# Kernel optimization log

Measured on AMD Instinct MI355X. Metric: run time of the kernel, lower is better.

The kernel has to match this reference:

```python
import jax, jax.numpy as jnp
import numpy as np
from jax import lax

SEQ, F, H1, H2, B, WV, OBJ, REL, VOCAB = 33, 20480, 900, 900, 2, 100, 35, 82, 117


def setup_inputs() -> dict:
    key = jax.random.key(0)
    ks = jax.random.split(key, 17)
    s = lambda k, shape: jax.random.normal(k, shape, jnp.float32) * 0.02
    return dict(
        x=jax.random.normal(ks[0], (SEQ, B, F), jnp.float32),
        w_ih1=s(ks[1], (4 * H1, F)), w_hh1=s(ks[2], (4 * H1, H1)),
        b_ih1=s(ks[3], (4 * H1,)), b_hh1=s(ks[4], (4 * H1,)),
        w_ih2=s(ks[5], (SEQ, 4 * H2, H1 + WV)), w_hh2=s(ks[6], (SEQ, 4 * H2, H2)),
        b_ih2=s(ks[7], (SEQ, 4 * H2)), b_hh2=s(ks[8], (SEQ, 4 * H2)),
        w_obj1=s(ks[9], (OBJ, H2)), b_obj1=s(ks[10], (OBJ,)),
        w_rel=s(ks[11], (REL, H2)), b_rel=s(ks[12], (REL,)),
        w_obj2=s(ks[13], (OBJ, H2)), b_obj2=s(ks[14], (OBJ,)),
        embed=s(ks[15], (VOCAB, WV)),
    )


def lstm_cell(xt, h, c, w_ih, w_hh, b_ih, b_hh):
    # torch gate order: input, forget, cell(g), output
    gates = xt @ w_ih.T + h @ w_hh.T + b_ih + b_hh
    i, f, g, o = jnp.split(gates, 4, axis=-1)
    c = jax.nn.sigmoid(f) * c + jax.nn.sigmoid(i) * jnp.tanh(g)
    h = jax.nn.sigmoid(o) * jnp.tanh(c)
    return h, c


def reference(x, w_ih1, w_hh1, b_ih1, b_hh1, w_ih2, w_hh2, b_ih2, b_hh2,
              w_obj1, b_obj1, w_rel, b_rel, w_obj2, b_obj2, embed):
    batch = x.shape[1]
    # layer-1 LSTM over full sequence
    def step1(carry, xt):
        h, c = lstm_cell(xt, carry[0], carry[1], w_ih1, w_hh1, b_ih1, b_hh1)
        return (h, c), h
    h0 = jnp.zeros((batch, H1), x.dtype)
    _, out1 = lax.scan(step1, (h0, h0), x)  # [SEQ, B, H1]

    # layer-2: first SEQ-2 cells with zero word vector, distinct weights per step
    wv0 = jnp.zeros((batch, WV), x.dtype)
    def step2(carry, inp):
        xt, wih, whh, bih, bhh = inp
        h, c = lstm_cell(jnp.concatenate([xt, wv0], axis=1), carry[0], carry[1], wih, whh, bih, bhh)
        return (h, c), None
    h20 = jnp.zeros((batch, H2), x.dtype)
    (h2, c2), _ = lax.scan(step2, (h20, h20),
                           (out1[:SEQ - 2], w_ih2[:SEQ - 2], w_hh2[:SEQ - 2],
                            b_ih2[:SEQ - 2], b_hh2[:SEQ - 2]))

    obj1 = h2 @ w_obj1.T + b_obj1                      # [B, 35]
    wv = embed[jnp.argmax(obj1, axis=1)]               # [B, 100]
    h2, c2 = lstm_cell(jnp.concatenate([out1[SEQ - 2], wv], axis=1), h2, c2,
                       w_ih2[SEQ - 2], w_hh2[SEQ - 2], b_ih2[SEQ - 2], b_hh2[SEQ - 2])

    rel = h2 @ w_rel.T + b_rel                         # [B, 82]
    wv = embed[jnp.argmax(rel, axis=1) + OBJ]
    h2, c2 = lstm_cell(jnp.concatenate([out1[SEQ - 1], wv], axis=1), h2, c2,
                       w_ih2[SEQ - 1], w_hh2[SEQ - 1], b_ih2[SEQ - 1], b_hh2[SEQ - 1])

    obj2 = h2 @ w_obj2.T + b_obj2                      # [B, 35]
    return (obj1, rel, obj2)
```

## Files before the change

### kernel.cpp

```cpp
#include <hip/hip_runtime.h>

#define SEQn 33
#define Fn   20480
#define Hn   900
#define Bn   2
#define WVn  100
#define OBJn 35
#define RELn 82
#define G4n  3600
#define Mn   66
#define NBLK 225

#define KS1  16
#define KSL1 (Fn/KS1)
#define RB1  15
#define RPB1 240
#define NC1  (KSL1/32)
#define WSTR 40

typedef __attribute__((ext_vector_type(8))) short bf16x8;
typedef __attribute__((ext_vector_type(4))) float f32x4;

__device__ __forceinline__ float sigf(float v){ return 1.f/(1.f+expf(-v)); }
__device__ __forceinline__ float dot4(float4 a, float4 b){ return a.x*b.x+a.y*b.y+a.z*b.z+a.w*b.w; }
__device__ __forceinline__ float wred(float v){
  #pragma unroll
  for (int d = 32; d >= 1; d >>= 1) v += __shfl_xor(v, d, 64);
  return v;
}
__device__ __forceinline__ float gload(const float* p){
  return __hip_atomic_load((const float*)p, __ATOMIC_RELAXED, __HIP_MEMORY_SCOPE_AGENT);
}
__device__ __forceinline__ void gstore(float* p, float v){
  __hip_atomic_store(p, v, __ATOMIC_RELAXED, __HIP_MEMORY_SCOPE_AGENT);
}
__device__ __forceinline__ unsigned short f2bf(float f){
  unsigned u = __float_as_uint(f);
  unsigned r = u + 0x7FFFu + ((u >> 16) & 1u);
  return (unsigned short)(r >> 16);
}
__device__ __forceinline__ float bf2f(unsigned short h){
  return __uint_as_float(((unsigned)h) << 16);
}

__device__ __forceinline__ void gbar(unsigned* bar){
  __syncthreads();
  if (threadIdx.x == 0) {
    unsigned g = __hip_atomic_load(&bar[0], __ATOMIC_RELAXED, __HIP_MEMORY_SCOPE_AGENT);
    unsigned cnt = __hip_atomic_fetch_add(&bar[32], 1u, __ATOMIC_RELAXED, __HIP_MEMORY_SCOPE_AGENT);
    if (cnt == (unsigned)(NBLK-1)) {
      __hip_atomic_store(&bar[32], 0u, __ATOMIC_RELAXED, __HIP_MEMORY_SCOPE_AGENT);
      asm volatile("s_waitcnt vmcnt(0)" ::: "memory");
      __hip_atomic_store(&bar[0], g+1u, __ATOMIC_RELAXED, __HIP_MEMORY_SCOPE_AGENT);
    } else {
      unsigned cur;
      do { __builtin_amdgcn_s_sleep(1);
           cur = __hip_atomic_load(&bar[0], __ATOMIC_RELAXED, __HIP_MEMORY_SCOPE_AGENT);
      } while (cur == g);
    }
  }
  __syncthreads();
}

__device__ __forceinline__ void gbar_lite(unsigned* bar, int wv){
  asm volatile("" ::: "memory");
  if (wv == 0) asm volatile("s_waitcnt vmcnt(0)" ::: "memory");
  __builtin_amdgcn_sched_barrier(0);
  __builtin_amdgcn_s_barrier();
  __builtin_amdgcn_sched_barrier(0);
  if (threadIdx.x == 0) {
    unsigned g = __hip_atomic_load(&bar[0], __ATOMIC_RELAXED, __HIP_MEMORY_SCOPE_AGENT);
    unsigned cnt = __hip_atomic_fetch_add(&bar[32], 1u, __ATOMIC_RELAXED, __HIP_MEMORY_SCOPE_AGENT);
    if (cnt == (unsigned)(NBLK-1)) {
      __hip_atomic_store(&bar[32], 0u, __ATOMIC_RELAXED, __HIP_MEMORY_SCOPE_AGENT);
      asm volatile("s_waitcnt vmcnt(0)" ::: "memory");
      __hip_atomic_store(&bar[0], g+1u, __ATOMIC_RELAXED, __HIP_MEMORY_SCOPE_AGENT);
    } else {
      unsigned cur;
      do { __builtin_amdgcn_s_sleep(1);
           cur = __hip_atomic_load(&bar[0], __ATOMIC_RELAXED, __HIP_MEMORY_SCOPE_AGENT);
      } while (cur == g);
    }
  }
  __builtin_amdgcn_sched_barrier(0);
  __builtin_amdgcn_s_barrier();
  __builtin_amdgcn_sched_barrier(0);
  asm volatile("" ::: "memory");
}

__global__ __launch_bounds__(320) void k1_mfma(
    const float* __restrict__ x, const float* __restrict__ w1,
    float* __restrict__ G1, unsigned* __restrict__ bar)
{
  const int tid = threadIdx.x;
  if (blockIdx.x == 0 && tid == 0) {
    __hip_atomic_store(&bar[0], 0u, __ATOMIC_RELAXED, __HIP_MEMORY_SCOPE_AGENT);
    __hip_atomic_store(&bar[32], 0u, __ATOMIC_RELAXED, __HIP_MEMORY_SCOPE_AGENT);
  }
  __shared__ unsigned short WhL[2][RPB1*WSTR], WlL[2][RPB1*WSTR];
  __shared__ unsigned short XhL[2][80*WSTR],  XlL[2][80*WSTR];

  const int rb = blockIdx.x % RB1;
  const int ks = blockIdx.x / RB1;
  const int r0 = rb * RPB1;
  const int kofs = ks * KSL1;
  const int wv_ = tid >> 6;
  const int lane = tid & 63;
  const int p = lane & 15;
  const int q = lane >> 4;

  f32x4 acc[3][5];
  #pragma unroll
  for (int rt = 0; rt < 3; ++rt)
    #pragma unroll
    for (int mt = 0; mt < 5; ++mt) acc[rt][mt] = (f32x4){0.f,0.f,0.f,0.f};

  float4 wr[6], xrg[2];

  #define ISSUE_STAGE(cc)                                                      \
    { const int kbase = kofs + (cc)*32;                                        \
      _Pragma("unroll")                                                        \
      for (int u = 0; u < 6; ++u) {                                            \
        const int idx = tid + u*320;                                           \
        const int row = idx >> 3, k4 = idx & 7;                                \
        wr[u] = *(const float4*)(w1 + (size_t)(r0+row)*Fn + kbase + k4*4);     \
      }                                                                        \
      _Pragma("unroll")                                                        \
      for (int u = 0; u < 2; ++u) {                                            \
        const int idx = tid + u*320;                                           \
        const int mrow = idx >> 3, k4 = idx & 7;                               \
        xrg[u] = (mrow < Mn)                                                   \
          ? *(const float4*)(x + (size_t)mrow*Fn + kbase + k4*4)               \
          : make_float4(0.f,0.f,0.f,0.f);                                      \
      }                                                                        \
    }

  #define CVTW(dsth, dstl, off, v)                                             \
    { const unsigned short h0=f2bf(v.x), h1=f2bf(v.y), h2=f2bf(v.z), h3=f2bf(v.w); \
      const unsigned short l0=f2bf(v.x-bf2f(h0)), l1=f2bf(v.y-bf2f(h1));       \
      const unsigned short l2=f2bf(v.z-bf2f(h2)), l3=f2bf(v.w-bf2f(h3));       \
      *(uint2*)&dsth[off] = make_uint2((unsigned)h0|((unsigned)h1<<16),        \
                                       (unsigned)h2|((unsigned)h3<<16));       \
      *(uint2*)&dstl[off] = make_uint2((unsigned)l0|((unsigned)l1<<16),        \
                                       (unsigned)l2|((unsigned)l3<<16));       \
    }

  #define WRITE_STAGE(bb)                                                     \
    { _Pragma("unroll")                                                       \
      for (int u = 0; u < 6; ++u) {                                           \
        const int idx = tid + u*320;                                          \
        const int row = idx >> 3, k4 = idx & 7;                               \
        CVTW(WhL[bb], WlL[bb], row*WSTR + k4*4, wr[u]);                       \
      }                                                                       \
      _Pragma("unroll")                                                       \
      for (int u = 0; u < 2; ++u) {                                           \
        const int idx = tid + u*320;                                          \
        const int mrow = idx >> 3, k4 = idx & 7;                              \
        CVTW(XhL[bb], XlL[bb], mrow*WSTR + k4*4, xrg[u]);                     \
      }                                                                       \
    }

  ISSUE_STAGE(0);
  WRITE_STAGE(0);
  __syncthreads();

  for (int c = 0; c < NC1; ++c) {
    const int buf = c & 1;
    if (c+1 < NC1) ISSUE_STAGE(c+1);

    bf16x8 Bh[5], Bl[5];
    #pragma unroll
    for (int mt = 0; mt < 5; ++mt) {
      const int moff = (mt*16 + p)*WSTR + q*8;
      Bh[mt] = *(const bf16x8*)&XhL[buf][moff];
      Bl[mt] = *(const bf16x8*)&XlL[buf][moff];
    }
    #pragma unroll
    for (int rt = 0; rt < 3; ++rt) {
      const int roff = ((wv_ + 5*rt)*16 + p)*WSTR + q*8;
      const bf16x8 Ah = *(const bf16x8*)&WhL[buf][roff];
      const bf16x8 Al = *(const bf16x8*)&WlL[buf][roff];
      #pragma unroll
      for (int mt = 0; mt < 5; ++mt) {
        acc[rt][mt] = __builtin_amdgcn_mfma_f32_16x16x32_bf16(Ah, Bh[mt], acc[rt][mt], 0, 0, 0);
        acc[rt][mt] = __builtin_amdgcn_mfma_f32_16x16x32_bf16(Ah, Bl[mt], acc[rt][mt], 0, 0, 0);
        acc[rt][mt] = __builtin_amdgcn_mfma_f32_16x16x32_bf16(Al, Bh[mt], acc[rt][mt], 0, 0, 0);
      }
    }

    if (c+1 < NC1) WRITE_STAGE(buf^1);
    __syncthreads();
  }

  #pragma unroll
  for (int rt = 0; rt < 3; ++rt)
    #pragma unroll
    for (int mt = 0; mt < 5; ++mt) {
      const int m = mt*16 + p;
      if (m < Mn) {
        #pragma unroll
        for (int r4 = 0; r4 < 4; ++r4) {
          const int grow = r0 + (wv_ + 5*rt)*16 + q*4 + r4;
          atomicAdd(&G1[(size_t)grow*Mn + m], acc[rt][mt][r4]);
        }
      }
    }
  #undef ISSUE_STAGE
  #undef WRITE_STAGE
  #undef CVTW
}

__global__ __launch_bounds__(512) void k_rec(
    const float* __restrict__ G1, float* __restrict__ out1, float* __restrict__ h2arr,
    const float* __restrict__ whh1,
    const float* __restrict__ wih2, const float* __restrict__ whh2,
    const float* __restrict__ bih2, const float* __restrict__ bhh2,
    const float* __restrict__ bih1, const float* __restrict__ bhh1,
    const float* __restrict__ wobj1, const float* __restrict__ bobj1,
    const float* __restrict__ wrel,  const float* __restrict__ brel,
    const float* __restrict__ wobj2, const float* __restrict__ bobj2,
    const float* __restrict__ embed, float* __restrict__ dout,
    unsigned* __restrict__ bar)
{
  __shared__ float hls[Bn][904];
  __shared__ float h2l[Bn][904];
  __shared__ float wvls[Bn][104];
  __shared__ float gls[16][68];
  __shared__ float bls[SEQn][16];
  __shared__ float gexA[16][Bn], gexB[16][Bn];
  __shared__ float cA[4][Bn], cB[4][Bn];
  __shared__ float red[4];
  __shared__ int idxls[Bn];

  const int tid = threadIdx.x;
  const int blk = blockIdx.x;
  const int j0 = blk * 4;
  const int wv_ = tid >> 6;
  const int lane = tid & 63;

  if (tid < 8) {
    const int jj = tid >> 1, m = tid & 1;
    cA[jj][m] = 0.f; cB[jj][m] = 0.f;
    gstore(h2arr + ((size_t)0*Bn + m)*Hn + j0 + jj, 0.f);
  }

  for (int qq = tid; qq < 16*Mn; qq += 512) {
    const int rho = qq / Mn, t = qq % Mn;
    const int gate = rho >> 2, jj = rho & 3;
    const size_t rA = (size_t)gate*Hn + j0 + jj;
    gls[rho][t] = G1[rA*Mn + t] + bih1[rA] + bhh1[rA];
  }
  for (int qq = tid; qq < SEQn*16; qq += 512) {
    const int s = qq / 16, rho = qq % 16;
    const int gate = rho >> 2, jj = rho & 3;
    const size_t ro = (size_t)s*G4n + (size_t)gate*Hn + j0 + jj;
    bls[s][rho] = bih2[ro] + bhh2[ro];
  }

  float4 wAreg[2][4];
  #pragma unroll
  for (int ri = 0; ri < 2; ++ri) {
    const int rho = wv_*2 + ri;
    const int gate = rho >> 2, jj = rho & 3;
    const size_t row = (size_t)gate*Hn + j0 + jj;
    #pragma unroll
    for (int e = 0; e < 4; ++e) {
      const int k = lane*4 + e*256;
      wAreg[ri][e] = (k <= Hn-4) ? *(const float4*)(whh1 + row*Hn + k)
                                 : make_float4(0.f,0.f,0.f,0.f);
    }
  }

  float4 wiR[2][4], whR[2][4];
  #define ISSUE_W(sp, KMX)                                                   \
    { _Pragma("unroll")                                                      \
      for (int ri = 0; ri < 2; ++ri) {                                       \
        const int rho = wv_*2 + ri;                                          \
        const int gate = rho >> 2, jj = rho & 3;                             \
        const size_t ro = (size_t)(sp)*G4n + (size_t)gate*Hn + j0 + jj;      \
        const float* wI = wih2 + ro*1000;                                    \
        const float* wH = whh2 + ro*Hn;                                      \
        _Pragma("unroll")                                                    \
        for (int e = 0; e < 4; ++e) {                                        \
          const int k = lane*4 + e*256;                                      \
          if (k <= (KMX)) wiR[ri][e] = *(const float4*)(wI + k);             \
          if (k <= 896)   whR[ri][e] = *(const float4*)(wH + k);             \
        }                                                                    \
      }                                                                      \
    }

  #define UPD_A(ivar)                                                        \
    { const float cc = sigf(gexA[4+jj][m])*cA[jj][m]                         \
                     + sigf(gexA[jj][m])*tanhf(gexA[8+jj][m]);               \
      cA[jj][m] = cc;                                                        \
      gstore(out1 + ((size_t)(ivar)*Bn + m)*Hn + j0 + jj,                    \
             sigf(gexA[12+jj][m])*tanhf(cc)); }

  #define UPD_B(svar)                                                        \
    { const float cc = sigf(gexB[4+jj][m])*cB[jj][m]                         \
                     + sigf(gexB[jj][m])*tanhf(gexB[8+jj][m]);               \
      cB[jj][m] = cc;                                                        \
      gstore(h2arr + ((size_t)((svar)+1)*Bn + m)*Hn + j0 + jj,               \
             sigf(gexB[12+jj][m])*tanhf(cc)); }

  ISSUE_W(0, 896);
  __syncthreads();

  if (lane == 0) {
    #pragma unroll
    for (int ri = 0; ri < 2; ++ri) {
      const int rho = wv_*2 + ri;
      gexA[rho][0] = gls[rho][0];
      gexA[rho][1] = gls[rho][1];
    }
  }
  __syncthreads();
  if (tid < 8) { const int jj = tid >> 1, m = tid & 1; UPD_A(0); }
  gbar(bar);

  for (int iv = 1; iv <= 31; ++iv) {
    const int s = iv - 1;
    float4 hv[2][4], h2v[2][4];
    #pragma unroll
    for (int e = 0; e < 4; ++e) {
      const int k = lane*4 + e*256;
      #pragma unroll
      for (int m = 0; m < 2; ++m) {
        hv[m][e]  = (k <= 896) ? *(const float4*)(out1  + ((size_t)s*Bn + m)*Hn + k)
                               : make_float4(0.f,0.f,0.f,0.f);
        h2v[m][e] = (k <= 896) ? *(const float4*)(h2arr + ((size_t)s*Bn + m)*Hn + k)
                               : make_float4(0.f,0.f,0.f,0.f);
      }
    }
    #pragma unroll
    for (int ri = 0; ri < 2; ++ri) {
      const int rho = wv_*2 + ri;
      float a0=0.f, a1=0.f, b0=0.f, b1=0.f;
      #pragma unroll
      for (int e = 0; e < 4; ++e) {
        const int k = lane*4 + e*256;
        if (k <= 896) {
          a0 += dot4(wAreg[ri][e], hv[0][e]);  a1 += dot4(wAreg[ri][e], hv[1][e]);
          b0 += dot4(wiR[ri][e],   hv[0][e]);  b1 += dot4(wiR[ri][e],   hv[1][e]);
          b0 += dot4(whR[ri][e],  h2v[0][e]);  b1 += dot4(whR[ri][e],  h2v[1][e]);
        }
      }
      a0 = wred(a0); a1 = wred(a1); b0 = wred(b0); b1 = wred(b1);
      if (lane == 0) {
        gexA[rho][0] = a0 + gls[rho][iv*Bn + 0];
        gexA[rho][1] = a1 + gls[rho][iv*Bn + 1];
        const float bb = bls[s][rho];
        gexB[rho][0] = b0 + bb;
        gexB[rho][1] = b1 + bb;
      }
    }
    asm volatile("s_waitcnt lgkmcnt(0)" ::: "memory");
    __builtin_amdgcn_sched_barrier(0);
    ISSUE_W(iv, (iv >= 31) ? 996 : 896);
    __builtin_amdgcn_sched_barrier(0);
    __builtin_amdgcn_s_barrier();
    __builtin_amdgcn_sched_barrier(0);
    if (tid < 8) {
      const int jj = tid >> 1, m = tid & 1;
      UPD_A(iv);
      UPD_B(s);
    }
    gbar_lite(bar, wv_);
  }

  for (int i = 32; i < 37; ++i) {
    if (i == 33 || i == 35) {
      if (wv_ < 2) {
        const int m = wv_;
        const int nout = (i == 33) ? OBJn : RELn;
        const int off = (i == 33) ? 0 : Bn*OBJn;
        float v = -1e30f; int idx = 0;
        for (int o = lane; o < nout; o += 64) {
          float t = gload(dout + off + m*nout + o);
          if (t > v) { v = t; idx = o; }
        }
        #pragma unroll
        for (int d = 32; d >= 1; d >>= 1) {
          float ov = __shfl_xor(v, d, 64);
          int   oi = __shfl_xor(idx, d, 64);
          if (ov > v || (ov == v && oi < idx)) { v = ov; idx = oi; }
        }
        if (lane == 0) idxls[m] = idx + ((i == 35) ? OBJn : 0);
      }
      __syncthreads();
      for (int qq = tid; qq < Bn*104; qq += 512) {
        const int m = qq / 104, v4 = qq % 104;
        wvls[m][v4] = (v4 < WVn) ? embed[(size_t)idxls[m]*WVn + v4] : 0.f;
      }
      __syncthreads();
    }

    const bool hasA = (i == 32);
    const int  s = (i == 33) ? 31 : (i == 35) ? 32 : -1;
    const bool hasB = (s >= 0);
    const int  srcA = (i == 35) ? 32 : i-1;

    if (hasA || i == 35) {
      for (int qq = tid; qq < 1808; qq += 512) {
        const int m = qq / 904, kk = qq % 904;
        hls[m][kk] = (kk < 900)
          ? gload(out1 + ((size_t)srcA*Bn + m)*Hn + kk) : 0.f;
      }
    }
    if (hasB) {
      for (int qq = tid; qq < 1808; qq += 512) {
        const int m = qq / 904, kk = qq % 904;
        h2l[m][kk] = (kk < 900)
          ? gload(h2arr + ((size_t)s*Bn + m)*Hn + kk) : 0.f;
      }
    }
    __syncthreads();

    if (hasA) {
      #pragma unroll
      for (int ri = 0; ri < 2; ++ri) {
        const int rho = wv_*2 + ri;
        float a0 = 0.f, a1 = 0.f;
        #pragma unroll
        for (int e = 0; e < 4; ++e) {
          const int k = lane*4 + e*256;
          if (k <= Hn-4) {
            a0 += dot4(wAreg[ri][e], *(const float4*)&hls[0][k]);
            a1 += dot4(wAreg[ri][e], *(const float4*)&hls[1][k]);
          }
        }
        a0 = wred(a0); a1 = wred(a1);
        if (lane == 0) {
          gexA[rho][0] = a0 + gls[rho][32*Bn + 0];
          gexA[rho][1] = a1 + gls[rho][32*Bn + 1];
        }
      }
    }

    if (hasB) {
      #pragma unroll
      for (int ri = 0; ri < 2; ++ri) {
        const int rho = wv_*2 + ri;
        float b0 = 0.f, b1 = 0.f;
        #pragma unroll
        for (int e = 0; e < 4; ++e) {
          const int k = lane*4 + e*256;
          if (k <= 896) {
            b0 += dot4(wiR[ri][e], *(const float4*)&hls[0][k]);
            b1 += dot4(wiR[ri][e], *(const float4*)&hls[1][k]);
            b0 += dot4(whR[ri][e], *(const float4*)&h2l[0][k]);
            b1 += dot4(whR[ri][e], *(const float4*)&h2l[1][k]);
          } else if (k >= 900 && k <= 996) {
            b0 += dot4(wiR[ri][e], *(const float4*)&wvls[0][k-900]);
            b1 += dot4(wiR[ri][e], *(const float4*)&wvls[1][k-900]);
          }
        }
        b0 = wred(b0); b1 = wred(b1);
        if (lane == 0) {
          const float bb = bls[s][rho];
          gexB[rho][0] = b0 + bb;
          gexB[rho][1] = b1 + bb;
        }
      }
      if (i == 33) ISSUE_W(32, 996);
    }

    if (i == 32 || i == 34 || i == 36) {
      const int nout = (i == 34) ? RELn : OBJn;
      const float* wh  = (i == 32) ? wobj1 : (i == 34) ? wrel : wobj2;
      const float* bh_ = (i == 32) ? bobj1 : (i == 34) ? brel : bobj2;
      const int off = (i == 32) ? 0 : (i == 34) ? (Bn*OBJn) : (Bn*OBJn + Bn*RELn);
      const int hb = (i == 32) ? 31 : (i == 34) ? 32 : 33;
      if (blk < nout*Bn) {
        const int o = blk >> 1, m = blk & 1;
        float p = 0.f;
        if (tid < 225) {
          const float4 wv4 = *(const float4*)(wh + (size_t)o*Hn + tid*4);
          const float* hp = h2arr + ((size_t)hb*Bn + m)*Hn + tid*4;
          p = wv4.x*gload(hp+0) + wv4.y*gload(hp+1)
            + wv4.z*gload(hp+2) + wv4.w*gload(hp+3);
        }
        if (wv_ < 4) {
          const float pr = wred(p);
          if (lane == 0) red[wv_] = pr;
        }
        __syncthreads();
        if (tid == 0)
          gstore(&dout[off + m*nout + o], red[0]+red[1]+red[2]+red[3] + bh_[o]);
      }
    }

    __syncthreads();
    if (tid < 8) {
      const int jj = tid >> 1, m = tid & 1;
      if (hasA) UPD_A(32);
      if (i == 33) UPD_B(31);
      if (i == 35) UPD_B(32);
    }

    if (i < 36) gbar(bar);
  }
  #undef ISSUE_W
  #undef UPD_A
  #undef UPD_B
}

extern "C" void kernel_launch(void* const* d_in, const int* in_sizes, int n_in,
                              void* d_out, int out_size, void* d_ws, size_t ws_size,
                              hipStream_t stream)
{
  (void)in_sizes; (void)n_in; (void)out_size; (void)ws_size;
  const float* x     = (const float*)d_in[0];
  const float* wih1  = (const float*)d_in[1];
  const float* whh1  = (const float*)d_in[2];
  const float* bih1  = (const float*)d_in[3];
  const float* bhh1  = (const float*)d_in[4];
  const float* wih2  = (const float*)d_in[5];
  const float* whh2  = (const float*)d_in[6];
  const float* bih2  = (const float*)d_in[7];
  const float* bhh2  = (const float*)d_in[8];
  const float* wobj1 = (const float*)d_in[9];
  const float* bobj1 = (const float*)d_in[10];
  const float* wrel  = (const float*)d_in[11];
  const float* brel  = (const float*)d_in[12];
  const float* wobj2 = (const float*)d_in[13];
  const float* bobj2 = (const float*)d_in[14];
  const float* embed = (const float*)d_in[15];
  float* dout = (float*)d_out;

  float* ws = (float*)d_ws;
  float* G1    = ws;
  float* out1  = G1 + (size_t)G4n*Mn;
  float* h2arr = out1 + (size_t)SEQn*Bn*Hn;
  unsigned* bar = (unsigned*)(h2arr + (size_t)34*Bn*Hn);

  hipMemsetAsync(G1, 0, (size_t)G4n*Mn*sizeof(float), stream);
  hipLaunchKernelGGL(k1_mfma, dim3(RB1*KS1), dim3(320), 0, stream, x, wih1, G1, bar);

  void* args[19];
  args[0]  = (void*)&G1;    args[1]  = (void*)&out1;  args[2]  = (void*)&h2arr;
  args[3]  = (void*)&whh1;  args[4]  = (void*)&wih2;  args[5]  = (void*)&whh2;
  args[6]  = (void*)&bih2;  args[7]  = (void*)&bhh2;  args[8]  = (void*)&bih1;
  args[9]  = (void*)&bhh1;  args[10] = (void*)&wobj1; args[11] = (void*)&bobj1;
  args[12] = (void*)&wrel;  args[13] = (void*)&brel;  args[14] = (void*)&wobj2;
  args[15] = (void*)&bobj2; args[16] = (void*)&embed; args[17] = (void*)&dout;
  args[18] = (void*)&bar;
  hipLaunchCooperativeKernel((void*)k_rec, dim3(NBLK), dim3(512), args, 0, stream);
}
```

Baseline: 500.2 us.

## Use hierarchical grid barrier and retile layer-1 GEMM into smaller blocks

The grid barrier now counts arrivals in 8 group counters, each on its own cache line, and only the last block of each group touches a top-level counter. This spreads the atomic contention that came from 225 blocks hitting one counter. Separately, the input-projection GEMM kernel now uses 144-row tiles with 192 threads (3 waves) instead of 240 rows with 320 threads, which gives 400 blocks for better CU coverage. The cost is more atomicAdd traffic on G1 and more x re-staging per block.

Result: faster. 475.7 us (-4.9%).

```diff
diff --git a/kernel.cpp b/kernel.cpp
--- a/kernel.cpp
+++ b/kernel.cpp
@@ -13,10 +13,11 @@
 
 #define KS1  16
 #define KSL1 (Fn/KS1)
-#define RB1  15
-#define RPB1 240
+#define RB1  25
+#define RPB1 144
 #define NC1  (KSL1/32)
 #define WSTR 40
+#define THR1 192
 
 typedef __attribute__((ext_vector_type(8))) short bf16x8;
 typedef __attribute__((ext_vector_type(4))) float f32x4;
@@ -43,22 +44,32 @@
   return __uint_as_float(((unsigned)h) << 16);
 }
 
+__device__ __forceinline__ void arrive_and_wait(unsigned* bar){
+  unsigned g = __hip_atomic_load(&bar[0], __ATOMIC_RELAXED, __HIP_MEMORY_SCOPE_AGENT);
+  const unsigned grp = (unsigned)blockIdx.x & 7u;
+  const unsigned gsz = (grp == 0u) ? 29u : 28u;
+  unsigned c = __hip_atomic_fetch_add(&bar[32 + grp*16], 1u, __ATOMIC_RELAXED, __HIP_MEMORY_SCOPE_AGENT);
+  if (c == gsz - 1u) {
+    unsigned c2 = __hip_atomic_fetch_add(&bar[16], 1u, __ATOMIC_RELAXED, __HIP_MEMORY_SCOPE_AGENT);
+    if (c2 == 7u) {
+      __hip_atomic_store(&bar[16], 0u, __ATOMIC_RELAXED, __HIP_MEMORY_SCOPE_AGENT);
+      #pragma unroll
+      for (int g8 = 0; g8 < 8; ++g8)
+        __hip_atomic_store(&bar[32 + g8*16], 0u, __ATOMIC_RELAXED, __HIP_MEMORY_SCOPE_AGENT);
+      asm volatile("s_waitcnt vmcnt(0)" ::: "memory");
+      __hip_atomic_store(&bar[0], g + 1u, __ATOMIC_RELAXED, __HIP_MEMORY_SCOPE_AGENT);
+      return;
+    }
+  }
+  unsigned cur;
+  do { __builtin_amdgcn_s_sleep(1);
+       cur = __hip_atomic_load(&bar[0], __ATOMIC_RELAXED, __HIP_MEMORY_SCOPE_AGENT);
+  } while (cur == g);
+}
+
 __device__ __forceinline__ void gbar(unsigned* bar){
   __syncthreads();
-  if (threadIdx.x == 0) {
-    unsigned g = __hip_atomic_load(&bar[0], __ATOMIC_RELAXED, __HIP_MEMORY_SCOPE_AGENT);
-    unsigned cnt = __hip_atomic_fetch_add(&bar[32], 1u, __ATOMIC_RELAXED, __HIP_MEMORY_SCOPE_AGENT);
-    if (cnt == (unsigned)(NBLK-1)) {
-      __hip_atomic_store(&bar[32], 0u, __ATOMIC_RELAXED, __HIP_MEMORY_SCOPE_AGENT);
-      asm volatile("s_waitcnt vmcnt(0)" ::: "memory");
-      __hip_atomic_store(&bar[0], g+1u, __ATOMIC_RELAXED, __HIP_MEMORY_SCOPE_AGENT);
-    } else {
-      unsigned cur;
-      do { __builtin_amdgcn_s_sleep(1);
-           cur = __hip_atomic_load(&bar[0], __ATOMIC_RELAXED, __HIP_MEMORY_SCOPE_AGENT);
-      } while (cur == g);
-    }
-  }
+  if (threadIdx.x == 0) arrive_and_wait(bar);
   __syncthreads();
 }
 
@@ -68,34 +79,22 @@
   __builtin_amdgcn_sched_barrier(0);
   __builtin_amdgcn_s_barrier();
   __builtin_amdgcn_sched_barrier(0);
-  if (threadIdx.x == 0) {
-    unsigned g = __hip_atomic_load(&bar[0], __ATOMIC_RELAXED, __HIP_MEMORY_SCOPE_AGENT);
-    unsigned cnt = __hip_atomic_fetch_add(&bar[32], 1u, __ATOMIC_RELAXED, __HIP_MEMORY_SCOPE_AGENT);
-    if (cnt == (unsigned)(NBLK-1)) {
-      __hip_atomic_store(&bar[32], 0u, __ATOMIC_RELAXED, __HIP_MEMORY_SCOPE_AGENT);
-      asm volatile("s_waitcnt vmcnt(0)" ::: "memory");
-      __hip_atomic_store(&bar[0], g+1u, __ATOMIC_RELAXED, __HIP_MEMORY_SCOPE_AGENT);
-    } else {
-      unsigned cur;
-      do { __builtin_amdgcn_s_sleep(1);
-           cur = __hip_atomic_load(&bar[0], __ATOMIC_RELAXED, __HIP_MEMORY_SCOPE_AGENT);
-      } while (cur == g);
-    }
-  }
+  if (threadIdx.x == 0) arrive_and_wait(bar);
   __builtin_amdgcn_sched_barrier(0);
   __builtin_amdgcn_s_barrier();
   __builtin_amdgcn_sched_barrier(0);
   asm volatile("" ::: "memory");
 }
 
-__global__ __launch_bounds__(320) void k1_mfma(
+__global__ __launch_bounds__(THR1) void k1_mfma(
     const float* __restrict__ x, const float* __restrict__ w1,
     float* __restrict__ G1, unsigned* __restrict__ bar)
 {
   const int tid = threadIdx.x;
-  if (blockIdx.x == 0 && tid == 0) {
-    __hip_atomic_store(&bar[0], 0u, __ATOMIC_RELAXED, __HIP_MEMORY_SCOPE_AGENT);
-    __hip_atomic_store(&bar[32], 0u, __ATOMIC_RELAXED, __HIP_MEMORY_SCOPE_AGENT);
+  if (blockIdx.x == 0 && tid < 10) {
+    if (tid == 0) __hip_atomic_store(&bar[0], 0u, __ATOMIC_RELAXED, __HIP_MEMORY_SCOPE_AGENT);
+    else if (tid == 1) __hip_atomic_store(&bar[16], 0u, __ATOMIC_RELAXED, __HIP_MEMORY_SCOPE_AGENT);
+    else __hip_atomic_store(&bar[32 + (tid-2)*16], 0u, __ATOMIC_RELAXED, __HIP_MEMORY_SCOPE_AGENT);
   }
   __shared__ unsigned short WhL[2][RPB1*WSTR], WlL[2][RPB1*WSTR];
   __shared__ unsigned short XhL[2][80*WSTR],  XlL[2][80*WSTR];
@@ -115,21 +114,21 @@
     #pragma unroll
     for (int mt = 0; mt < 5; ++mt) acc[rt][mt] = (f32x4){0.f,0.f,0.f,0.f};
 
-  float4 wr[6], xrg[2];
+  float4 wr[6], xrg[4];
 
   #define ISSUE_STAGE(cc)                                                      \
     { const int kbase = kofs + (cc)*32;                                        \
       _Pragma("unroll")                                                        \
       for (int u = 0; u < 6; ++u) {                                            \
-        const int idx = tid + u*320;                                           \
+        const int idx = tid + u*THR1;                                          \
         const int row = idx >> 3, k4 = idx & 7;                                \
         wr[u] = *(const float4*)(w1 + (size_t)(r0+row)*Fn + kbase + k4*4);     \
       }                                                                        \
       _Pragma("unroll")                                                        \
-      for (int u = 0; u < 2; ++u) {                                            \
-        const int idx = tid + u*320;                                           \
+      for (int u = 0; u < 4; ++u) {                                            \
+        const int idx = tid + u*THR1;                                          \
         const int mrow = idx >> 3, k4 = idx & 7;                               \
-        xrg[u] = (mrow < Mn)                                                   \
+        xrg[u] = (idx < 640 && mrow < Mn)                                      \
           ? *(const float4*)(x + (size_t)mrow*Fn + kbase + k4*4)               \
           : make_float4(0.f,0.f,0.f,0.f);                                      \
       }                                                                        \
@@ -148,15 +147,17 @@
   #define WRITE_STAGE(bb)                                                     \
     { _Pragma("unroll")                                                       \
       for (int u = 0; u < 6; ++u) {                                           \
-        const int idx = tid + u*320;                                          \
+        const int idx = tid + u*THR1;                                         \
         const int row = idx >> 3, k4 = idx & 7;                               \
         CVTW(WhL[bb], WlL[bb], row*WSTR + k4*4, wr[u]);                       \
       }                                                                       \
       _Pragma("unroll")                                                       \
-      for (int u = 0; u < 2; ++u) {                                           \
-        const int idx = tid + u*320;                                          \
-        const int mrow = idx >> 3, k4 = idx & 7;                              \
-        CVTW(XhL[bb], XlL[bb], mrow*WSTR + k4*4, xrg[u]);                     \
+      for (int u = 0; u < 4; ++u) {                                           \
+        const int idx = tid + u*THR1;                                         \
+        if (idx < 640) {                                                      \
+          const int mrow = idx >> 3, k4 = idx & 7;                            \
+          CVTW(XhL[bb], XlL[bb], mrow*WSTR + k4*4, xrg[u]);                   \
+        }                                                                     \
       }                                                                       \
     }
 
@@ -177,7 +178,7 @@
     }
     #pragma unroll
     for (int rt = 0; rt < 3; ++rt) {
-      const int roff = ((wv_ + 5*rt)*16 + p)*WSTR + q*8;
+      const int roff = ((wv_ + 3*rt)*16 + p)*WSTR + q*8;
       const bf16x8 Ah = *(const bf16x8*)&WhL[buf][roff];
       const bf16x8 Al = *(const bf16x8*)&WlL[buf][roff];
       #pragma unroll
@@ -200,7 +201,7 @@
       if (m < Mn) {
         #pragma unroll
         for (int r4 = 0; r4 < 4; ++r4) {
-          const int grow = r0 + (wv_ + 5*rt)*16 + q*4 + r4;
+          const int grow = r0 + (wv_ + 3*rt)*16 + q*4 + r4;
           atomicAdd(&G1[(size_t)grow*Mn + m], acc[rt][mt][r4]);
         }
       }
@@ -535,7 +536,7 @@
   unsigned* bar = (unsigned*)(h2arr + (size_t)34*Bn*Hn);
 
   hipMemsetAsync(G1, 0, (size_t)G4n*Mn*sizeof(float), stream);
-  hipLaunchKernelGGL(k1_mfma, dim3(RB1*KS1), dim3(320), 0, stream, x, wih1, G1, bar);
+  hipLaunchKernelGGL(k1_mfma, dim3(RB1*KS1), dim3(THR1), 0, stream, x, wih1, G1, bar);
 
   void* args[19];
   args[0]  = (void*)&G1;    args[1]  = (void*)&out1;  args[2]  = (void*)&h2arr;
```
